# Kernel optimization log

Measured on AMD Instinct MI355X. Metric: run time of the kernel, lower is better.

## Reference

```python
import jax, jax.numpy as jnp
import numpy as np

B, T, C, H = 128, 256, 256, 8
HS = C // H  # 32
EPS = 1e-5


def _layernorm(x, g, b):
    mu = jnp.mean(x, axis=-1, keepdims=True)
    var = jnp.mean(jnp.square(x - mu), axis=-1, keepdims=True)
    return g * (x - mu) / jnp.sqrt(var + EPS) + b


def setup_inputs() -> dict:
    key = jax.random.key(0)
    ks = jax.random.split(key, 12)
    s = 0.02
    return {
        "x": jax.random.normal(ks[0], (B, T, C), dtype=jnp.float32),
        "Wk": jax.random.normal(ks[1], (H, C, HS), dtype=jnp.float32) * s,
        "Wq": jax.random.normal(ks[2], (H, C, HS), dtype=jnp.float32) * s,
        "Wv": jax.random.normal(ks[3], (H, C, HS), dtype=jnp.float32) * s,
        "Wp": jax.random.normal(ks[4], (C, C), dtype=jnp.float32) * s,
        "bp": jnp.zeros((C,), dtype=jnp.float32),
        "W1": jax.random.normal(ks[5], (C, 4 * C), dtype=jnp.float32) * s,
        "b1": jnp.zeros((4 * C,), dtype=jnp.float32),
        "W2": jax.random.normal(ks[6], (4 * C, C), dtype=jnp.float32) * s,
        "b2": jnp.zeros((C,), dtype=jnp.float32),
        "g1": jnp.ones((C,), dtype=jnp.float32),
        "be1": jnp.zeros((C,), dtype=jnp.float32),
        "g2": jnp.ones((C,), dtype=jnp.float32),
        "be2": jnp.zeros((C,), dtype=jnp.float32),
    }


def reference(x, Wk, Wq, Wv, Wp, bp, W1, b1, W2, b2, g1, be1, g2, be2):
    Bx, Tx, Cx = x.shape
    # --- multi-head self-attention on ln1(x) ---
    h = _layernorm(x, g1, be1)
    k = jnp.einsum('btc,hcd->bhtd', h, Wk)
    q = jnp.einsum('btc,hcd->bhtd', h, Wq)
    v = jnp.einsum('btc,hcd->bhtd', h, Wv)
    # NOTE: source computes k @ q^T (transposed vs standard) and scales by C**-0.5
    scores = jnp.einsum('bhtd,bhsd->bhts', k, q) * (Cx ** -0.5)
    mask = jnp.tril(jnp.ones((Tx, Tx), dtype=bool))  # causal lower-triangular
    scores = jnp.where(mask, scores, -jnp.inf)
    w = jax.nn.softmax(scores, axis=-1)
    o = jnp.einsum('bhts,bhsd->bhtd', w, v)
    o = o.transpose(0, 2, 1, 3).reshape(Bx, Tx, Cx)  # concat heads
    x = x + (o @ Wp + bp)
    # --- feed-forward (swish) on ln2(x) ---
    h2 = _layernorm(x, g2, be2)
    f = h2 @ W1 + b1
    f = f * jax.nn.sigmoid(f)  # swish
    f = f @ W2 + b2
    return x + f
```

## Files before the change

### kernel.cpp

```cpp
#include <hip/hip_runtime.h>
#include <cstdint>

#define BB 128
#define TT 256
#define CC 256
#define HH 8
#define HSZ 32
#define NT (BB*TT)
#define CF (4*CC)
#define LN_EPS 1e-5f
#define SCALE 0.0625f

typedef __attribute__((ext_vector_type(8))) __bf16 bf16x8;
typedef __attribute__((ext_vector_type(4))) float f32x4;
typedef __attribute__((ext_vector_type(16))) float f32x16;
typedef __attribute__((ext_vector_type(2))) long i64x2;
typedef unsigned short u16;
typedef unsigned int u32;
typedef unsigned char u8;

__device__ __forceinline__ u16 f2bf(float f) {
  u32 u = __float_as_uint(f);
  u32 r = (u + 0x7fffu + ((u >> 16) & 1u)) >> 16;
  return (u16)r;
}
__device__ __forceinline__ u8 f2f8(float f) {
  return (u8)(__builtin_amdgcn_cvt_pk_fp8_f32(f, f, 0, false) & 0xff);
}
__device__ __forceinline__ u32 f2f8x4(float a, float b, float c, float d) {
  u32 pk = (u32)__builtin_amdgcn_cvt_pk_fp8_f32(a, b, 0, false);
  return (u32)__builtin_amdgcn_cvt_pk_fp8_f32(c, d, (int)pk, true);
}
__device__ __forceinline__ int swz3i(int r) { return (r ^ (r >> 2)) & 3; }
__device__ __forceinline__ int pkrow(int row, int k) {
  int g = (k >> 4) & 3, h = (k >> 3) & 1, j = k & 7;
  int c = (h << 1) + (g >> 1);
  int cp = c ^ swz3i(row);
  return (k & ~63) + cp * 16 + ((g & 1) << 3) + j;
}

__device__ __forceinline__ void gload16(const void* g, void* l) {
  __builtin_amdgcn_global_load_lds(
      (const __attribute__((address_space(1))) u32*)(uintptr_t)g,
      (__attribute__((address_space(3))) u32*)(u32)(uintptr_t)l,
      16, 0, 0);
}

__device__ __forceinline__ void wait_vm0() {
  asm volatile("s_waitcnt vmcnt(0)" ::: "memory");
  __builtin_amdgcn_sched_barrier(0);
}
__device__ __forceinline__ void wait_vm4() {
  asm volatile("s_waitcnt vmcnt(4)" ::: "memory");
  __builtin_amdgcn_sched_barrier(0);
}
__device__ __forceinline__ void wait_vm8() {
  asm volatile("s_waitcnt vmcnt(8)" ::: "memory");
  __builtin_amdgcn_sched_barrier(0);
}
__device__ __forceinline__ void wait_vm4_lgkm0() {
  asm volatile("s_waitcnt vmcnt(4) lgkmcnt(0)" ::: "memory");
  __builtin_amdgcn_sched_barrier(0);
}
__device__ __forceinline__ void wait_vm0_lgkm0() {
  asm volatile("s_waitcnt vmcnt(0) lgkmcnt(0)" ::: "memory");
  __builtin_amdgcn_sched_barrier(0);
}
__device__ __forceinline__ void sbar() {
  __builtin_amdgcn_s_barrier();
  __builtin_amdgcn_sched_barrier(0);
}

__global__ __launch_bounds__(256) void conv_t(
    const float* __restrict__ Wk, const float* __restrict__ Wq,
    const float* __restrict__ Wv, const float* __restrict__ Wp,
    const float* __restrict__ W1, const float* __restrict__ W2,
    u8* __restrict__ WkqvT8, u8* __restrict__ WpT8,
    u8* __restrict__ W1T8, u8* __restrict__ W2T8) {
  __shared__ u8 ldsT[64][68];
  int bid = blockIdx.x, tid = threadIdx.x;
  int n0, k0, K;
  u8* dst;
  int mode;
  const float* src = nullptr;
  int sk = 0;
  if (bid < 48) {
    mode = 0; n0 = (bid >> 2) * 64; k0 = (bid & 3) * 64; K = 256; dst = WkqvT8;
  } else if (bid < 112) {
    int l = bid - 48;
    mode = 1; n0 = (l >> 2) * 64; k0 = (l & 3) * 64; K = 256; dst = W1T8;
    src = W1; sk = 1024;
  } else if (bid < 176) {
    int l = bid - 112;
    mode = 1; n0 = (l >> 4) * 64; k0 = (l & 15) * 64; K = 1024; dst = W2T8;
    src = W2; sk = 256;
  } else {
    int l = bid - 176;
    mode = 1; n0 = (l >> 2) * 64; k0 = (l & 3) * 64; K = 256; dst = WpT8;
    src = Wp; sk = 256;
  }
  int kr = tid >> 2;
  int nbase = (tid & 3) * 16;
#pragma unroll
  for (int u = 0; u < 4; ++u) {
    int nl = nbase + u * 4;
    int ng = n0 + nl;
    float4 v;
    if (mode == 0) {
      const float* W = (ng < 256) ? Wk : (ng < 512 ? Wq : Wv);
      int inner = ng & 255;
      v = *reinterpret_cast<const float4*>(
          &W[((inner >> 5) << 13) + (size_t)(k0 + kr) * 32 + (inner & 31)]);
    } else {
      v = *reinterpret_cast<const float4*>(
          &src[(size_t)(k0 + kr) * sk + ng]);
    }
    ldsT[nl + 0][kr] = f2f8(v.x);
    ldsT[nl + 1][kr] = f2f8(v.y);
    ldsT[nl + 2][kr] = f2f8(v.z);
    ldsT[nl + 3][kr] = f2f8(v.w);
  }
  __syncthreads();
  int nl = tid >> 2;
  int nglob = n0 + nl;
  int sz = swz3i(nglob);
  u8* drow = dst + (size_t)nglob * K + k0;
#pragma unroll
  for (int c4 = (tid & 3) * 4; c4 < (tid & 3) * 4 + 4; ++c4) {
    int q = c4 >> 1, s = c4 & 1;
    int kb = q * 8 + s * 4;
    u32 pk = (u32)ldsT[nl][kb] | ((u32)ldsT[nl][kb + 1] << 8) |
             ((u32)ldsT[nl][kb + 2] << 16) | ((u32)ldsT[nl][kb + 3] << 24);
    int g = (kb >> 4) & 3, h8 = (kb >> 3) & 1;
    int cp = ((h8 << 1) + (g >> 1)) ^ sz;
    *reinterpret_cast<u32*>(drow + cp * 16 + ((g & 1) << 3) + (kb & 7)) = pk;
  }
}

__global__ __launch_bounds__(256) void ln_kernel(const float* __restrict__ x,
                                                 const float* __restrict__ g,
                                                 const float* __restrict__ b,
                                                 u8* __restrict__ out) {
  int tid = threadIdx.x;
  int wid = tid >> 6, lane = tid & 63;
  int row = blockIdx.x * 4 + wid;
  const float4 v = reinterpret_cast<const float4*>(x + (size_t)row * CC)[lane];
  float s = v.x + v.y + v.z + v.w;
#pragma unroll
  for (int o = 32; o; o >>= 1) s += __shfl_xor(s, o, 64);
  float mu = s * (1.0f / CC);
  float dx = v.x - mu, dy = v.y - mu, dz = v.z - mu, dw = v.w - mu;
  float ss = dx * dx + dy * dy + dz * dz + dw * dw;
#pragma unroll
  for (int o = 32; o; o >>= 1) ss += __shfl_xor(ss, o, 64);
  float inv = rsqrtf(ss * (1.0f / CC) + LN_EPS);
  const float4 gv = reinterpret_cast<const float4*>(g)[lane];
  const float4 bv = reinterpret_cast<const float4*>(b)[lane];
  u32 pk = f2f8x4(gv.x * dx * inv + bv.x, gv.y * dy * inv + bv.y,
                  gv.z * dz * inv + bv.z, gv.w * dw * inv + bv.w);
  *reinterpret_cast<u32*>(out + (size_t)row * CC + pkrow(row, lane * 4)) = pk;
}

template <int EPI>
__device__ __forceinline__ void epi_store(f32x4 v, int m, int n,
                                          const float* bias,
                                          const float* resid, void* outp,
                                          int N) {
  size_t off = (size_t)m * N + n;
  if (EPI == 0) {
    u16 pk[4];
#pragma unroll
    for (int r = 0; r < 4; ++r) pk[r] = f2bf(v[r]);
    *reinterpret_cast<uint2*>(&((u16*)outp)[off]) = *reinterpret_cast<uint2*>(pk);
  } else if (EPI == 1) {
    const float4 bv = *reinterpret_cast<const float4*>(&bias[n]);
    const float4 rv = *reinterpret_cast<const float4*>(&resid[off]);
    float4 o;
    o.x = v[0] + bv.x + rv.x;
    o.y = v[1] + bv.y + rv.y;
    o.z = v[2] + bv.z + rv.z;
    o.w = v[3] + bv.w + rv.w;
    *reinterpret_cast<float4*>(&((float*)outp)[off]) = o;
  }
}

template <int NB, int EPI>
__global__ __launch_bounds__(512, 4) void panel_fused(
    const u8* __restrict__ Asrc, const u8* __restrict__ WT8,
    const float* __restrict__ bias, const float* __restrict__ resid,
    void* __restrict__ outp, int N) {
  __shared__ u8 Bw[4][256][64];
  int tid = threadIdx.x;
  int w = tid >> 6, lane = tid & 63;
  int l32 = lane & 31, h = lane >> 5;
  int th = w >> 2, fq = w & 3;
  int m0 = blockIdx.x * 64;

#define STAGEP(nb)                                                            \
  {                                                                           \
    _Pragma("unroll") for (int it = 0; it < 8; ++it) {                        \
      int f = it * 512 + tid;                                                 \
      int kg = f >> 10, t = (f >> 2) & 255, c = f & 3;                        \
      gload16(WT8 + (size_t)((nb) * 256 + t) * 256 + kg * 64 + c * 16,        \
              &Bw[0][0][0] + f * 16);                                         \
    }                                                                         \
  }
  i64x2 aa[4][2];
  {
    int ar = th * 32 + l32;
    int az = swz3i(ar);
#pragma unroll
    for (int kg = 0; kg < 4; ++kg)
#pragma unroll
      for (int p = 0; p < 2; ++p)
        aa[kg][p] = *reinterpret_cast<const i64x2*>(
            Asrc + (size_t)(m0 + ar) * 256 + kg * 64 +
            ((((h << 1) + p) ^ az) << 4));
  }
  STAGEP(0);

#pragma unroll 1
  for (int nb = 0; nb < NB; ++nb) {
    if (nb == 0) wait_vm0(); else wait_vm8();
    sbar();
    f32x16 a1[2] = {};
#pragma unroll
    for (int kg = 0; kg < 4; ++kg) {
#pragma unroll
      for (int p = 0; p < 2; ++p) {
        i64x2 bB[2];
#pragma unroll
        for (int j = 0; j < 2; ++j) {
          int br = fq * 64 + j * 32 + l32, bz = swz3i(br);
          bB[j] = *reinterpret_cast<const i64x2*>(
              &Bw[kg][br][(((h << 1) + p) ^ bz) << 4]);
        }
#pragma unroll
        for (int j = 0; j < 2; ++j) {
          a1[j] = __builtin_amdgcn_mfma_f32_32x32x16_fp8_fp8(
              bB[j][0], aa[kg][p][0], a1[j], 0, 0, 0);
          a1[j] = __builtin_amdgcn_mfma_f32_32x32x16_fp8_fp8(
              bB[j][1], aa[kg][p][1], a1[j], 0, 0, 0);
        }
      }
    }
    sbar();
    if (nb < NB - 1) STAGEP(nb + 1);
    int m = m0 + th * 32 + l32;
#pragma unroll
    for (int j = 0; j < 2; ++j) {
#pragma unroll
      for (int q = 0; q < 4; ++q) {
        int n = nb * 256 + fq * 64 + j * 32 + q * 8 + h * 4;
        f32x4 v = {a1[j][q * 4 + 0], a1[j][q * 4 + 1],
                   a1[j][q * 4 + 2], a1[j][q * 4 + 3]};
        epi_store<EPI>(v, m, n, bias, resid, outp, N);
      }
    }
  }
#undef STAGEP
}

__global__ __launch_bounds__(512, 4) void ffn_fused(
    const u8* __restrict__ hb, const u8* __restrict__ W1T8,
    const u8* __restrict__ W2T8, const float* __restrict__ b1,
    const float* __restrict__ b2, const float* __restrict__ x2,
    float* __restrict__ outp) {
  __shared__ u8 Bw1[4][128][64];
  __shared__ u8 Bw2[2][256][64];
  __shared__ u8 Ff[2][64][64];
  __shared__ float b1l[1024];
  int tid = threadIdx.x;
  int w = tid >> 6, lane = tid & 63;
  int l32 = lane & 31, h = lane >> 5;
  int th = w >> 2, fq = w & 3;
  int m0 = blockIdx.x * 64;

#define STAGE_W1(nb)                                                          \
  {                                                                           \
    _Pragma("unroll") for (int it = 0; it < 4; ++it) {                        \
      int f = it * 512 + tid;                                                 \
      int kg = f >> 9, t = (f >> 2) & 127, c = f & 3;                         \
      gload16(W1T8 + (size_t)((nb) * 128 + t) * 256 + kg * 64 + c * 16,       \
              &Bw1[0][0][0] + f * 16);                                        \
    }                                                                         \
  }
#define STAGE_W2(nb)                                                          \
  {                                                                           \
    _Pragma("unroll") for (int it = 0; it < 4; ++it) {                        \
      int f = it * 512 + tid;                                                 \
      int kg2 = f >> 10, o = (f >> 2) & 255, c = f & 3;                       \
      gload16(W2T8 + (size_t)o * 1024 + (nb) * 128 + kg2 * 64 + c * 16,       \
              &Bw2[0][0][0] + f * 16);                                        \
    }                                                                         \
  }
  i64x2 aa[4][2];
  {
    int ar = th * 32 + l32;
    int az = swz3i(ar);
#pragma unroll
    for (int kg = 0; kg < 4; ++kg)
#pragma unroll
      for (int p = 0; p < 2; ++p)
        aa[kg][p] = *reinterpret_cast<const i64x2*>(
            hb + (size_t)(m0 + ar) * 256 + kg * 64 +
            ((((h << 1) + p) ^ az) << 4));
  }
  if (w < 4) gload16(b1 + (size_t)(w * 256 + lane * 4), b1l + w * 256 + lane * 4);
  STAGE_W1(0);
  STAGE_W2(0);

  f32x16 acc2[2] = {};
#pragma unroll 1
  for (int nb = 0; nb < 8; ++nb) {
    wait_vm4();
    sbar();
    f32x16 a1 = {};
#pragma unroll
    for (int kg = 0; kg < 4; ++kg) {
      int br = fq * 32 + l32, bz = swz3i(br);
#pragma unroll
      for (int p = 0; p < 2; ++p) {
        i64x2 bB = *reinterpret_cast<const i64x2*>(
            &Bw1[kg][br][(((h << 1) + p) ^ bz) << 4]);
        a1 = __builtin_amdgcn_mfma_f32_32x32x16_fp8_fp8(
            bB[0], aa[kg][p][0], a1, 0, 0, 0);
        a1 = __builtin_amdgcn_mfma_f32_32x32x16_fp8_fp8(
            bB[1], aa[kg][p][1], a1, 0, 0, 0);
      }
    }
    sbar();
    if (nb < 7) STAGE_W1(nb + 1);
    int kg2w = fq >> 1;
    {
      int t = th * 32 + l32;
      int tz = swz3i(t);
#pragma unroll
      for (int q = 0; q < 4; ++q) {
        int g = (fq & 1) * 2 + (q >> 1);
        int hh = q & 1;
        int c = (hh << 1) + (g >> 1);
        const float4 bv = *reinterpret_cast<const float4*>(
            &b1l[nb * 128 + fq * 32 + q * 8 + h * 4]);
        float bf[4] = {bv.x, bv.y, bv.z, bv.w};
        float sv[4];
#pragma unroll
        for (int r = 0; r < 4; ++r) {
          float fv = a1[q * 4 + r] + bf[r];
          float e = __builtin_amdgcn_exp2f(fv * -1.44269504f);
          sv[r] = fv * __builtin_amdgcn_rcpf(1.0f + e);
        }
        *reinterpret_cast<u32*>(
            &Ff[kg2w][t][((c ^ tz) << 4) + ((g & 1) << 3) + h * 4]) =
            f2f8x4(sv[0], sv[1], sv[2], sv[3]);
      }
    }
    if (nb < 7) wait_vm4_lgkm0();
    else        wait_vm0_lgkm0();
    sbar();
#pragma unroll
    for (int kg2 = 0; kg2 < 2; ++kg2)
#pragma unroll
      for (int p = 0; p < 2; ++p) {
        int ar2 = th * 32 + l32;
        i64x2 fa = *reinterpret_cast<const i64x2*>(
            &Ff[kg2][ar2][(((h << 1) + p) ^ swz3i(ar2)) << 4]);
        i64x2 bb2[2];
#pragma unroll
        for (int j = 0; j < 2; ++j) {
          int br = fq * 64 + j * 32 + l32;
          bb2[j] = *reinterpret_cast<const i64x2*>(
              &Bw2[kg2][br][(((h << 1) + p) ^ swz3i(br)) << 4]);
        }
#pragma unroll
        for (int j = 0; j < 2; ++j) {
          acc2[j] = __builtin_amdgcn_mfma_f32_32x32x16_fp8_fp8(
              bb2[j][0], fa[0], acc2[j], 0, 0, 0);
          acc2[j] = __builtin_amdgcn_mfma_f32_32x32x16_fp8_fp8(
              bb2[j][1], fa[1], acc2[j], 0, 0, 0);
        }
      }
    sbar();
    if (nb < 7) STAGE_W2(nb + 1);
  }
#undef STAGE_W1
#undef STAGE_W2
  int m = m0 + th * 32 + l32;
#pragma unroll
  for (int j = 0; j < 2; ++j) {
#pragma unroll
    for (int q = 0; q < 4; ++q) {
      int n = fq * 64 + j * 32 + q * 8 + h * 4;
      f32x4 v = {acc2[j][q * 4 + 0], acc2[j][q * 4 + 1],
                 acc2[j][q * 4 + 2], acc2[j][q * 4 + 3]};
      epi_store<1>(v, m, n, b2, x2, outp, CC);
    }
  }
}

__global__ __launch_bounds__(256) void attn_kernel(const u16* __restrict__ kqv,
                                                   u8* __restrict__ o8) {
  __shared__ u16 q_lds[256 * 32];
  __shared__ u16 vT[32 * 256];
  __shared__ u16 pT[4 * 16 * 64];
  int bh = blockIdx.x;
  int b = bh >> 3, h = bh & 7;
  int tid = threadIdx.x, wid = tid >> 6, lane = tid & 63;
  int l16 = lane & 15, lh = lane >> 4;
  const size_t rowbase = (size_t)b * TT * 768;
  {
    int sr = tid >> 2, c = tid & 3;
    for (int s = sr; s < 256; s += 64) {
      uint4 qv = *reinterpret_cast<const uint4*>(
          &kqv[rowbase + (size_t)s * 768 + 256 + h * 32 + c * 8]);
      *reinterpret_cast<uint4*>((char*)q_lds + ((s * 64 + c * 16) ^ ((s & 7) << 4))) = qv;
      u16 tmp[8];
      *reinterpret_cast<uint4*>(tmp) = *reinterpret_cast<const uint4*>(
          &kqv[rowbase + (size_t)s * 768 + 512 + h * 32 + c * 8]);
#pragma unroll
      for (int dd = 0; dd < 8; ++dd) {
        int e = dd ^ c;
        int d = c * 8 + e;
        vT[d * 256 + (((s >> 3) ^ (d & 7)) << 3) + (s & 7)] = tmp[e];
      }
    }
  }
  __syncthreads();
  u16* pw = &pT[wid * 16 * 64];
  const float C1 = 0.09016844f;
  for (int j = 0; j < 4; ++j) {
    int t16 = (j * 4 + wid) * 16;
    bf16x8 kb = *reinterpret_cast<const bf16x8*>(
        &kqv[rowbase + (size_t)(t16 + l16) * 768 + h * 32 + lh * 8]);
    float m2 = -3e38f, lsum = 0.f;
    f32x4 oacc[2] = {};
    for (int st = 0; st <= j; ++st) {
      int s0 = st << 6;
      float v[4][4];
#pragma unroll
      for (int sj = 0; sj < 4; ++sj) {
        int srow = s0 + sj * 16 + l16;
        bf16x8 qa = *reinterpret_cast<const bf16x8*>(
            (char*)q_lds + ((srow * 64 + lh * 16) ^ ((srow & 7) << 4)));
        f32x4 z = {0.f, 0.f, 0.f, 0.f};
        f32x4 sc = __builtin_amdgcn_mfma_f32_16x16x32_bf16(qa, kb, z, 0, 0, 0);
#pragma unroll
        for (int r = 0; r < 4; ++r) {
          float val = sc[r] * C1;
          if (st == j) {
            if (sj * 16 + lh * 4 + r > wid * 16 + l16) val = -1e30f;
          }
          v[sj][r] = val;
        }
      }
      float mx = v[0][0];
#pragma unroll
      for (int sj = 0; sj < 4; ++sj)
#pragma unroll
        for (int r = 0; r < 4; ++r) mx = fmaxf(mx, v[sj][r]);
      mx = fmaxf(mx, __shfl_xor(mx, 16, 64));
      mx = fmaxf(mx, __shfl_xor(mx, 32, 64));
      float mn = fmaxf(m2, mx);
      float alpha = exp2f(m2 - mn);
      m2 = mn;
      float rs = 0.f;
#pragma unroll
      for (int sj = 0; sj < 4; ++sj) {
        u16 pk[4];
#pragma unroll
        for (int r = 0; r < 4; ++r) {
          float p = exp2f(v[sj][r] - mn);
          rs += p;
          pk[r] = f2bf(p);
        }
        *reinterpret_cast<uint2*>(
            (char*)pw + ((l16 * 128 + sj * 32 + lh * 8) ^ ((l16 & 7) << 4))) =
            *reinterpret_cast<const uint2*>(pk);
      }
      rs += __shfl_xor(rs, 16, 64);
      rs += __shfl_xor(rs, 32, 64);
      lsum = lsum * alpha + rs;
#pragma unroll
      for (int r = 0; r < 4; ++r) {
        float a = __shfl(alpha, (lane & 48) | (lh * 4 + r), 64);
        oacc[0][r] *= a;
        oacc[1][r] *= a;
      }
#pragma unroll
      for (int ks = 0; ks < 2; ++ks) {
        bf16x8 pa = *reinterpret_cast<const bf16x8*>(
            (char*)pw + ((l16 * 128 + ks * 64 + lh * 16) ^ ((l16 & 7) << 4)));
#pragma unroll
        for (int nI = 0; nI < 2; ++nI) {
          int d = nI * 16 + l16;
          int sch = ((s0 + ks * 32 + lh * 8) >> 3) ^ (d & 7);
          bf16x8 vb = *reinterpret_cast<const bf16x8*>(&vT[d * 256 + (sch << 3)]);
          oacc[nI] = __builtin_amdgcn_mfma_f32_16x16x32_bf16(pa, vb, oacc[nI], 0, 0, 0);
        }
      }
    }
#pragma unroll
    for (int r = 0; r < 4; ++r) {
      float ls = __shfl(lsum, (lane & 48) | (lh * 4 + r), 64);
      float inv = 1.0f / ls;
      int t = t16 + lh * 4 + r;
      size_t rb = (size_t)(b * TT + t) * CC;
#pragma unroll
      for (int nI = 0; nI < 2; ++nI) {
        int c = h * HSZ + nI * 16 + l16;
        o8[rb + pkrow(t, c)] = f2f8(oacc[nI][r] * inv);
      }
    }
  }
}

extern "C" void kernel_launch(void* const* d_in, const int* in_sizes, int n_in,
                              void* d_out, int out_size, void* d_ws, size_t ws_size,
                              hipStream_t stream) {
  const float* x   = (const float*)d_in[0];
  const float* Wk  = (const float*)d_in[1];
  const float* Wq  = (const float*)d_in[2];
  const float* Wv  = (const float*)d_in[3];
  const float* Wp  = (const float*)d_in[4];
  const float* bp  = (const float*)d_in[5];
  const float* W1  = (const float*)d_in[6];
  const float* b1  = (const float*)d_in[7];
  const float* W2  = (const float*)d_in[8];
  const float* b2  = (const float*)d_in[9];
  const float* g1  = (const float*)d_in[10];
  const float* be1 = (const float*)d_in[11];
  const float* g2  = (const float*)d_in[12];
  const float* be2 = (const float*)d_in[13];

  char* ws = (char*)d_ws;
  u16* kqv = (u16*)(ws + 0);
  u8*  o8  = (u8*)(ws + 50331648);
  float* x2 = (float*)(ws + 67108864);
  u8*  hb  = (u8*)(ws + 100663296);
  char* wb = ws + 117440512;
  u8*  WkqvT8 = (u8*)(wb);
  u8*  WpT8   = (u8*)(wb + 196608);
  u8*  W1T8   = (u8*)(wb + 196608 + 65536);
  u8*  W2T8   = (u8*)(wb + 196608 + 65536 + 262144);

  conv_t<<<192, 256, 0, stream>>>(Wk, Wq, Wv, Wp, W1, W2,
                                  WkqvT8, WpT8, W1T8, W2T8);
  ln_kernel<<<NT / 4, 256, 0, stream>>>(x, g1, be1, hb);
  panel_fused<3, 0><<<NT / 64, 512, 0, stream>>>(
      hb, WkqvT8, nullptr, nullptr, kqv, 768);
  attn_kernel<<<BB * HH, 256, 0, stream>>>(kqv, o8);
  panel_fused<1, 1><<<NT / 64, 512, 0, stream>>>(
      o8, WpT8, bp, x, x2, 256);
  ln_kernel<<<NT / 4, 256, 0, stream>>>(x2, g2, be2, hb);
  ffn_fused<<<NT / 64, 512, 0, stream>>>(hb, W1T8, W2T8, b1, b2, x2, (float*)d_out);
}
```

Baseline: 145.9 us.

## Replace online softmax with two-pass full-row softmax in attention kernel

Computes all score tiles for a query block into registers first, takes one max over the full causal row, then does exp and P·V in a single pass without rescaling. This drops the per-tile alpha rescale, the shuffles and the running max/sum bookkeeping. Key fragments are now preloaded for all four iterations before the barrier, and launch bounds request 4 blocks per CU. The cost is higher register pressure from holding up to 16 score fragments, which could spill under the tighter occupancy bound.

```diff
diff --git a/kernel.cpp b/kernel.cpp
--- a/kernel.cpp
+++ b/kernel.cpp
@@ -398,8 +398,8 @@
   }
 }
 
-__global__ __launch_bounds__(256) void attn_kernel(const u16* __restrict__ kqv,
-                                                   u8* __restrict__ o8) {
+__global__ __launch_bounds__(256, 4) void attn_kernel(
+    const u16* __restrict__ kqv, u8* __restrict__ o8) {
   __shared__ u16 q_lds[256 * 32];
   __shared__ u16 vT[32 * 256];
   __shared__ u16 pT[4 * 16 * 64];
@@ -425,66 +425,69 @@
       }
     }
   }
+  bf16x8 kb[4];
+#pragma unroll
+  for (int jj = 0; jj < 4; ++jj) {
+    int t16 = (jj * 4 + wid) * 16;
+    kb[jj] = *reinterpret_cast<const bf16x8*>(
+        &kqv[rowbase + (size_t)(t16 + l16) * 768 + h * 32 + lh * 8]);
+  }
   __syncthreads();
   u16* pw = &pT[wid * 16 * 64];
   const float C1 = 0.09016844f;
   for (int j = 0; j < 4; ++j) {
     int t16 = (j * 4 + wid) * 16;
-    bf16x8 kb = *reinterpret_cast<const bf16x8*>(
-        &kqv[rowbase + (size_t)(t16 + l16) * 768 + h * 32 + lh * 8]);
-    float m2 = -3e38f, lsum = 0.f;
-    f32x4 oacc[2] = {};
-    for (int st = 0; st <= j; ++st) {
+    f32x4 sc[4][4];
+#pragma unroll
+    for (int st = 0; st < 4; ++st) {
+      if (st > j) continue;
       int s0 = st << 6;
-      float v[4][4];
 #pragma unroll
       for (int sj = 0; sj < 4; ++sj) {
         int srow = s0 + sj * 16 + l16;
         bf16x8 qa = *reinterpret_cast<const bf16x8*>(
             (char*)q_lds + ((srow * 64 + lh * 16) ^ ((srow & 7) << 4)));
         f32x4 z = {0.f, 0.f, 0.f, 0.f};
-        f32x4 sc = __builtin_amdgcn_mfma_f32_16x16x32_bf16(qa, kb, z, 0, 0, 0);
+        sc[st][sj] = __builtin_amdgcn_mfma_f32_16x16x32_bf16(qa, kb[j], z, 0, 0, 0);
+      }
+    }
+    float pm[4] = {-3e38f, -3e38f, -3e38f, -3e38f};
+#pragma unroll
+    for (int st = 0; st < 4; ++st) {
+      if (st > j) continue;
+#pragma unroll
+      for (int sj = 0; sj < 4; ++sj)
 #pragma unroll
         for (int r = 0; r < 4; ++r) {
-          float val = sc[r] * C1;
+          float val = sc[st][sj][r] * C1;
           if (st == j) {
             if (sj * 16 + lh * 4 + r > wid * 16 + l16) val = -1e30f;
           }
-          v[sj][r] = val;
-        }
-      }
-      float mx = v[0][0];
-#pragma unroll
-      for (int sj = 0; sj < 4; ++sj)
-#pragma unroll
-        for (int r = 0; r < 4; ++r) mx = fmaxf(mx, v[sj][r]);
-      mx = fmaxf(mx, __shfl_xor(mx, 16, 64));
-      mx = fmaxf(mx, __shfl_xor(mx, 32, 64));
-      float mn = fmaxf(m2, mx);
-      float alpha = exp2f(m2 - mn);
-      m2 = mn;
-      float rs = 0.f;
+          sc[st][sj][r] = val;
+          pm[sj] = fmaxf(pm[sj], val);
+        }
+    }
+    float mx = fmaxf(fmaxf(pm[0], pm[1]), fmaxf(pm[2], pm[3]));
+    mx = fmaxf(mx, __shfl_xor(mx, 16, 64));
+    mx = fmaxf(mx, __shfl_xor(mx, 32, 64));
+    float rs = 0.f;
+    f32x4 oacc[2] = {};
+#pragma unroll
+    for (int st = 0; st < 4; ++st) {
+      if (st > j) continue;
+      int s0 = st << 6;
 #pragma unroll
       for (int sj = 0; sj < 4; ++sj) {
         u16 pk[4];
 #pragma unroll
         for (int r = 0; r < 4; ++r) {
-          float p = exp2f(v[sj][r] - mn);
+          float p = exp2f(sc[st][sj][r] - mx);
           rs += p;
           pk[r] = f2bf(p);
         }
         *reinterpret_cast<uint2*>(
             (char*)pw + ((l16 * 128 + sj * 32 + lh * 8) ^ ((l16 & 7) << 4))) =
             *reinterpret_cast<const uint2*>(pk);
-      }
-      rs += __shfl_xor(rs, 16, 64);
-      rs += __shfl_xor(rs, 32, 64);
-      lsum = lsum * alpha + rs;
-#pragma unroll
-      for (int r = 0; r < 4; ++r) {
-        float a = __shfl(alpha, (lane & 48) | (lh * 4 + r), 64);
-        oacc[0][r] *= a;
-        oacc[1][r] *= a;
       }
 #pragma unroll
       for (int ks = 0; ks < 2; ++ks) {
@@ -499,9 +502,11 @@
         }
       }
     }
+    rs += __shfl_xor(rs, 16, 64);
+    rs += __shfl_xor(rs, 32, 64);
 #pragma unroll
     for (int r = 0; r < 4; ++r) {
-      float ls = __shfl(lsum, (lane & 48) | (lh * 4 + r), 64);
+      float ls = __shfl(rs, (lane & 48) | (lh * 4 + r), 64);
       float inv = 1.0f / ls;
       int t = t16 + lh * 4 + r;
       size_t rb = (size_t)(b * TT + t) * CC;
```

New measurement: 167.9 us. 15.1% more time.
